# Optimization experiments

Measured on AMD Instinct MI355X. Metric: run time of the kernel, lower is better.

The kernel has to match this reference:

```python
import jax, jax.numpy as jnp
import numpy as np

D_MODEL = 1024
N_HEADS = 16
D_HEAD = D_MODEL // N_HEADS
D_FF = 4096
EPS = 1e-5


def layer_norm(x, g, b):
    mu = jnp.mean(x, axis=-1, keepdims=True)
    var = jnp.mean(jnp.square(x - mu), axis=-1, keepdims=True)
    return (x - mu) * jax.lax.rsqrt(var + EPS) * g + b


def setup_inputs() -> dict:
    key = jax.random.key(0)
    ks = jax.random.split(key, 8)
    s = 1.0 / np.sqrt(D_MODEL)
    return {
        "x": jax.random.normal(ks[0], (2, 2048, D_MODEL), dtype=jnp.float32),
        "Wq": jax.random.normal(ks[1], (N_HEADS, D_MODEL, D_HEAD), dtype=jnp.float32) * s,
        "Wk": jax.random.normal(ks[2], (N_HEADS, D_MODEL, D_HEAD), dtype=jnp.float32) * s,
        "Wv": jax.random.normal(ks[3], (N_HEADS, D_MODEL, D_HEAD), dtype=jnp.float32) * s,
        "Wo": jax.random.normal(ks[4], (D_MODEL, D_MODEL), dtype=jnp.float32) * s,
        "bo": jnp.zeros((D_MODEL,), dtype=jnp.float32),
        "ln1_g": jnp.ones((D_MODEL,), dtype=jnp.float32),
        "ln1_b": jnp.zeros((D_MODEL,), dtype=jnp.float32),
        "ln2_g": jnp.ones((D_MODEL,), dtype=jnp.float32),
        "ln2_b": jnp.zeros((D_MODEL,), dtype=jnp.float32),
        "W1": jax.random.normal(ks[5], (D_MODEL, D_FF), dtype=jnp.float32) * s,
        "b1": jnp.zeros((D_FF,), dtype=jnp.float32),
        "W2": jax.random.normal(ks[6], (D_FF, D_MODEL), dtype=jnp.float32) * (1.0 / np.sqrt(D_FF)),
        "b2": jnp.zeros((D_MODEL,), dtype=jnp.float32),
    }


def reference(x, Wq, Wk, Wv, Wo, bo, ln1_g, ln1_b, ln2_g, ln2_b, W1, b1, W2, b2):
    # Pre-norm MHA (per-head projections batched over head axis h)
    xn = layer_norm(x, ln1_g, ln1_b)
    q = jnp.einsum("bsd,hde->bhse", xn, Wq)
    k = jnp.einsum("bsd,hde->bhse", xn, Wk)
    v = jnp.einsum("bsd,hde->bhse", xn, Wv)
    scores = jnp.einsum("bhqe,bhke->bhqk", q, k) / jnp.sqrt(jnp.float32(D_HEAD))
    w = jax.nn.softmax(scores, axis=-1)
    attn = jnp.einsum("bhqk,bhke->bhqe", w, v)  # [b,h,s,dh]
    b, h, s, dh = attn.shape
    concat = attn.transpose(0, 2, 1, 3).reshape(b, s, h * dh)  # head concat order matches torch cat
    attn_out = concat @ Wo + bo
    hidden = x + attn_out
    hn = layer_norm(hidden, ln2_g, ln2_b)
    ff = jax.nn.gelu(hn @ W1 + b1, approximate=False) @ W2 + b2  # torch nn.GELU default = exact
    return hidden + ff
```

## Files before the change

kernel.cpp:

```cpp
#include <hip/hip_runtime.h>
#include <hip/hip_bf16.h>

typedef __bf16 bf16;
typedef __bf16 bf16x4 __attribute__((ext_vector_type(4)));
typedef __bf16 bf16x8 __attribute__((ext_vector_type(8)));
typedef float  f32x4  __attribute__((ext_vector_type(4)));

static __device__ __forceinline__ f32x4 mfma16(bf16x8 a, bf16x8 b, f32x4 c) {
  return __builtin_amdgcn_mfma_f32_16x16x32_bf16(a, b, c, 0, 0, 0);
}

static __device__ __forceinline__ float fexp2(float x) {
  return __builtin_amdgcn_exp2f(x);
}

static __device__ __forceinline__ void gl_lds16(const bf16* g, bf16* l) {
  __builtin_amdgcn_global_load_lds(
      (const __attribute__((address_space(1))) void*)g,
      (__attribute__((address_space(3))) void*)l, 16, 0, 0);
}

struct TrTab {
  const float* src[6];
  bf16* dst[6];
  int R[6], C[6], ntx[6], nty[6];
  int base[7];
};

__global__ __launch_bounds__(256) void tr6_kernel(TrTab tab) {
  int bid = blockIdx.x;
  int j = 0;
  while (j < 5 && bid >= tab.base[j + 1]) ++j;
  const int local = bid - tab.base[j];
  const int R = tab.R[j], C = tab.C[j];
  const int ntx = tab.ntx[j];
  const int per_z = ntx * tab.nty[j];
  const int z = local / per_z;
  const int rem = local - z * per_z;
  const int by = rem / ntx, bx = rem - by * ntx;
  const float* in = tab.src[j];
  bf16* out = tab.dst[j];

  __shared__ bf16 tile[32][33];
  const size_t zoff = (size_t)z * R * C;
  const int tx = threadIdx.x & 31, ty = threadIdx.x >> 5;
  const int x = bx * 32 + tx;
  const int y0 = by * 32;
#pragma unroll
  for (int jj = 0; jj < 4; ++jj)
    tile[ty + jj * 8][tx] = (bf16)in[zoff + (size_t)(y0 + ty + jj * 8) * C + x];
  __syncthreads();
  const int x2 = y0 + tx;
  const int y2 = bx * 32;
#pragma unroll
  for (int jj = 0; jj < 4; ++jj)
    out[zoff + (size_t)(y2 + ty + jj * 8) * R + x2] = tile[tx][ty + jj * 8];
}

__global__ __launch_bounds__(256) void trb_kernel(const bf16* __restrict__ inp,
                                                  bf16* __restrict__ out,
                                                  int R, int C) {
  __shared__ bf16 tile[32][33];
  const size_t zoff = (size_t)blockIdx.z * R * C;
  const int tx = threadIdx.x & 31, ty = threadIdx.x >> 5;
  const int x = blockIdx.x * 32 + tx;
  const int y0 = blockIdx.y * 32;
#pragma unroll
  for (int j = 0; j < 4; ++j)
    tile[ty + j * 8][tx] = inp[zoff + (size_t)(y0 + ty + j * 8) * C + x];
  __syncthreads();
  const int x2 = y0 + tx;
  const int y2 = blockIdx.x * 32;
#pragma unroll
  for (int j = 0; j < 4; ++j)
    out[zoff + (size_t)(y2 + ty + j * 8) * R + x2] = tile[tx][ty + j * 8];
}

__global__ __launch_bounds__(256) void ln_kernel(const float* __restrict__ inp,
                                                 const float* __restrict__ g,
                                                 const float* __restrict__ bt,
                                                 bf16* __restrict__ outp) {
  const int row = blockIdx.x;
  const int t = threadIdx.x;
  f32x4 v = ((const f32x4*)inp)[row * 256 + t];
  float s = v[0] + v[1] + v[2] + v[3];
  float sq = v[0] * v[0] + v[1] * v[1] + v[2] * v[2] + v[3] * v[3];
#pragma unroll
  for (int off = 32; off > 0; off >>= 1) {
    s += __shfl_xor(s, off);
    sq += __shfl_xor(sq, off);
  }
  __shared__ float red[8];
  const int wave = t >> 6, lane = t & 63;
  if (lane == 0) {
    red[wave] = s;
    red[wave + 4] = sq;
  }
  __syncthreads();
  s = red[0] + red[1] + red[2] + red[3];
  sq = red[4] + red[5] + red[6] + red[7];
  const float mu = s * (1.0f / 1024.0f);
  const float var = sq * (1.0f / 1024.0f) - mu * mu;
  const float rstd = rsqrtf(fmaxf(var, 0.0f) + 1e-5f);
  f32x4 gg = ((const f32x4*)g)[t];
  f32x4 bb = ((const f32x4*)bt)[t];
  bf16 o[4];
#pragma unroll
  for (int i = 0; i < 4; ++i)
    o[i] = (bf16)((v[i] - mu) * rstd * gg[i] + bb[i]);
  *(uint2*)&outp[(size_t)row * 1024 + 4 * t] = *(uint2*)o;
}

enum { EPI_QKV = 0, EPI_O = 1, EPI_FF1 = 2, EPI_FF2 = 3 };

#define VMW(N) asm volatile("s_waitcnt vmcnt(" #N ")" ::: "memory")
#define BARR                        \
  do {                              \
    __builtin_amdgcn_s_barrier();   \
    asm volatile("" ::: "memory");  \
  } while (0)

template <int EPI>
__global__ __launch_bounds__(512) void gemm256(
    const bf16* __restrict__ A, const bf16* __restrict__ Bt, const int K,
    const float* __restrict__ bias, bf16* __restrict__ outB) {
  __shared__ __align__(16) bf16 sA[2][256 * 64];
  __shared__ __align__(16) bf16 sB[2][256 * 64];
  const int t = threadIdx.x;
  const int lane = t & 63, wave = t >> 6;
  const int quad = lane >> 4, l15 = lane & 15;
  const int wm = wave >> 2, wn = wave & 3;
  const int m0 = blockIdx.y * 256, n0 = blockIdx.x * 256;
  const int srow = lane >> 3;
  const int scol = ((lane & 7) ^ srow) * 8;
  const int bch = (wave & 3) + (wave >> 2) * 8;

  const bf16* aS0 = A + (size_t)(m0 + wave * 8 + srow) * K + scol;
  const bf16* aS1 = aS0 + (size_t)64 * K;
  const bf16* bS0 = Bt + (size_t)(n0 + bch * 8 + srow) * K + scol;
  const bf16* bS1 = bS0 + (size_t)32 * K;
  const size_t rsk = (size_t)128 * K;

  auto stA0 = [&](int buf, int ko) {
    gl_lds16(aS0 + ko, &sA[buf][wave * 512]);
    gl_lds16(aS0 + ko + rsk, &sA[buf][(wave + 16) * 512]);
  };
  auto stB0 = [&](int buf, int ko) {
    gl_lds16(bS0 + ko, &sB[buf][bch * 512]);
    gl_lds16(bS0 + ko + rsk, &sB[buf][(bch + 16) * 512]);
  };
  auto stB1 = [&](int buf, int ko) {
    gl_lds16(bS1 + ko, &sB[buf][(bch + 4) * 512]);
    gl_lds16(bS1 + ko + rsk, &sB[buf][(bch + 20) * 512]);
  };
  auto stA1 = [&](int buf, int ko) {
    gl_lds16(aS1 + ko, &sA[buf][(wave + 8) * 512]);
    gl_lds16(aS1 + ko + rsk, &sA[buf][(wave + 24) * 512]);
  };

  f32x4 acc[8][4];
#pragma unroll
  for (int i = 0; i < 8; ++i)
#pragma unroll
    for (int j = 0; j < 4; ++j) acc[i][j] = {0.f, 0.f, 0.f, 0.f};

  bf16x8 af[4][2], bf0[2][2], bf1[2][2];

  auto ldA = [&](int buf, int mh) {
#pragma unroll
    for (int i = 0; i < 4; ++i) {
      const int row = wm * 128 + mh * 64 + i * 16 + l15;
#pragma unroll
      for (int ks = 0; ks < 2; ++ks) {
        const int col = ((ks * 4 + quad) ^ (row & 7)) * 8;
        af[i][ks] = *(const bf16x8*)&sA[buf][row * 64 + col];
      }
    }
  };
  auto ldB = [&](int buf, int nh, bf16x8 (&bfm)[2][2]) {
#pragma unroll
    for (int j = 0; j < 2; ++j) {
      const int row = wn * 64 + nh * 32 + j * 16 + l15;
#pragma unroll
      for (int ks = 0; ks < 2; ++ks) {
        const int col = ((ks * 4 + quad) ^ (row & 7)) * 8;
        bfm[j][ks] = *(const bf16x8*)&sB[buf][row * 64 + col];
      }
    }
  };
  auto mm = [&](int mh, int nh, bf16x8 (&bfm)[2][2]) {
    asm volatile("s_waitcnt lgkmcnt(0)" ::: "memory");
    __builtin_amdgcn_sched_barrier(0);
    __builtin_amdgcn_s_setprio(1);
#pragma unroll
    for (int ks = 0; ks < 2; ++ks)
#pragma unroll
      for (int i = 0; i < 4; ++i)
#pragma unroll
        for (int j = 0; j < 2; ++j)
          acc[mh * 4 + i][nh * 2 + j] =
              mfma16(af[i][ks], bfm[j][ks], acc[mh * 4 + i][nh * 2 + j]);
    __builtin_amdgcn_s_setprio(0);
    __builtin_amdgcn_sched_barrier(0);
  };

  stA0(0, 0);
  stB0(0, 0);
  stB1(0, 0);
  stA1(0, 0);

  const int NT = K >> 6;
#pragma unroll 1
  for (int it = 0; it < NT - 1; ++it) {
    const int cur = it & 1, nxt = cur ^ 1;
    const int ko = (it + 1) * 64;
    VMW(4);
    BARR;
    ldA(cur, 0);
    ldB(cur, 0, bf0);
    stA0(nxt, ko);
    mm(0, 0, bf0);
    VMW(4);
    BARR;
    ldB(cur, 1, bf1);
    stB0(nxt, ko);
    mm(0, 1, bf1);
    VMW(4);
    BARR;
    ldA(cur, 1);
    stB1(nxt, ko);
    mm(1, 1, bf1);
    ldB(cur, 0, bf0);
    stA1(nxt, ko);
    mm(1, 0, bf0);
  }
  {
    const int cur = (NT - 1) & 1;
    VMW(4);
    BARR;
    ldA(cur, 0);
    ldB(cur, 0, bf0);
    mm(0, 0, bf0);
    VMW(2);
    BARR;
    ldB(cur, 1, bf1);
    mm(0, 1, bf1);
    VMW(0);
    BARR;
    ldA(cur, 1);
    mm(1, 1, bf1);
    ldB(cur, 0, bf0);
    mm(1, 0, bf0);
  }

#pragma unroll
  for (int ni = 0; ni < 4; ++ni) {
    const int n = n0 + wn * 64 + ni * 16 + l15;
    float bv = 0.f;
    if constexpr (EPI == EPI_FF1) bv = bias[n];
#pragma unroll
    for (int mi = 0; mi < 8; ++mi) {
#pragma unroll
      for (int r = 0; r < 4; ++r) {
        const int m = m0 + wm * 128 + mi * 16 + quad * 4 + r;
        float v = acc[mi][ni][r];
        if constexpr (EPI == EPI_QKV) {
          const int which = n >> 10, nn = n & 1023;
          const int h = nn >> 6, e = nn & 63;
          const int b = m >> 11, s2 = m & 2047;
          outB[(size_t)which * 4194304 +
               ((size_t)(b * 16 + h) * 2048 + s2) * 64 + e] = (bf16)v;
        } else {
          v += bv;
          v = 0.5f * v * (1.0f + erff(v * 0.70710678118654752f));
          outB[(size_t)m * 4096 + n] = (bf16)v;
        }
      }
    }
  }
}

template <int EPI, bool NARROW>
__global__ __launch_bounds__(256) void gemm_bt(
    const bf16* __restrict__ A, const bf16* __restrict__ Bt, const int K,
    const float* __restrict__ bias, const float* __restrict__ res,
    bf16* __restrict__ outB, float* __restrict__ outF) {
  constexpr int BN = NARROW ? 64 : 128;
  constexpr int NI = NARROW ? 2 : 4;
  constexpr int BCH = BN / 32;
  __shared__ __align__(16) bf16 sA[2][128 * 64];
  __shared__ __align__(16) bf16 sB[2][BN * 64];
  const int t = threadIdx.x;
  const int lane = t & 63, wave = t >> 6;
  const int quad = lane >> 4, l15 = lane & 15;
  const int wr = wave >> 1, wc = wave & 1;
  const int m0 = blockIdx.y * 128, n0 = blockIdx.x * BN;
  const int srow = lane >> 3;
  const int scol = ((lane & 7) ^ srow) * 8;

  const bf16* aPtr[4];
#pragma unroll
  for (int c = 0; c < 4; ++c)
    aPtr[c] = A + (size_t)(m0 + wave * 32 + c * 8 + srow) * K + scol;
  const bf16* bPtr[BCH];
#pragma unroll
  for (int c = 0; c < BCH; ++c)
    bPtr[c] = Bt + (size_t)(n0 + wave * (BCH * 8) + c * 8 + srow) * K + scol;

  f32x4 acc[4][NI];
#pragma unroll
  for (int i = 0; i < 4; ++i)
#pragma unroll
    for (int j = 0; j < NI; ++j) acc[i][j] = {0.f, 0.f, 0.f, 0.f};

  const int niter = K >> 6;
#pragma unroll
  for (int c = 0; c < 4; ++c)
    gl_lds16(aPtr[c], &sA[0][(wave * 4 + c) * 512]);
#pragma unroll
  for (int c = 0; c < BCH; ++c)
    gl_lds16(bPtr[c], &sB[0][(wave * BCH + c) * 512]);

  for (int it = 0; it < niter; ++it) {
    const int cur = it & 1, nxt = cur ^ 1;
    __syncthreads();
    if (it + 1 < niter) {
      const int off = (it + 1) * 64;
#pragma unroll
      for (int c = 0; c < 4; ++c)
        gl_lds16(aPtr[c] + off, &sA[nxt][(wave * 4 + c) * 512]);
#pragma unroll
      for (int c = 0; c < BCH; ++c)
        gl_lds16(bPtr[c] + off, &sB[nxt][(wave * BCH + c) * 512]);
    }
#pragma unroll
    for (int ks = 0; ks < 2; ++ks) {
      bf16x8 af[4], bfr[NI];
#pragma unroll
      for (int mi = 0; mi < 4; ++mi) {
        const int row = wr * 64 + mi * 16 + l15;
        const int col = ((ks * 4 + quad) ^ (row & 7)) * 8;
        af[mi] = *(const bf16x8*)&sA[cur][row * 64 + col];
      }
#pragma unroll
      for (int ni = 0; ni < NI; ++ni) {
        const int row = wc * (BN / 2) + ni * 16 + l15;
        const int col = ((ks * 4 + quad) ^ (row & 7)) * 8;
        bfr[ni] = *(const bf16x8*)&sB[cur][row * 64 + col];
      }
#pragma unroll
      for (int mi = 0; mi < 4; ++mi)
#pragma unroll
        for (int ni = 0; ni < NI; ++ni)
          acc[mi][ni] = mfma16(af[mi], bfr[ni], acc[mi][ni]);
    }
  }

#pragma unroll
  for (int mi = 0; mi < 4; ++mi) {
#pragma unroll
    for (int ni = 0; ni < NI; ++ni) {
      const int n = n0 + wc * (BN / 2) + ni * 16 + l15;
#pragma unroll
      for (int r = 0; r < 4; ++r) {
        const int m = m0 + wr * 64 + mi * 16 + quad * 4 + r;
        float v = acc[mi][ni][r];
        if constexpr (EPI == EPI_QKV) {
          const int which = n >> 10, nn = n & 1023;
          const int h = nn >> 6, e = nn & 63;
          const int b = m >> 11, s2 = m & 2047;
          outB[(size_t)which * 4194304 +
               ((size_t)(b * 16 + h) * 2048 + s2) * 64 + e] = (bf16)v;
        } else if constexpr (EPI == EPI_O) {
          v += bias[n] + res[(size_t)m * 1024 + n];
          outF[(size_t)m * 1024 + n] = v;
        } else if constexpr (EPI == EPI_FF1) {
          v += bias[n];
          v = 0.5f * v * (1.0f + erff(v * 0.70710678118654752f));
          outB[(size_t)m * 4096 + n] = (bf16)v;
        } else {
          v += bias[n] + res[(size_t)m * 1024 + n];
          outF[(size_t)m * 1024 + n] = v;
        }
      }
    }
  }
}

__global__ __launch_bounds__(512, 4) void attn_kernel(
    const bf16* __restrict__ q, const bf16* __restrict__ k,
    const bf16* __restrict__ vt, bf16* __restrict__ ao) {
  __shared__ __align__(16) bf16 sP[256 * 72];
  __shared__ __align__(16) bf16 sK[2][64 * 64];
  __shared__ __align__(16) bf16 sV[2][64 * 64];
  const int t = threadIdx.x;
  const int lane = t & 63, wave = t >> 6;
  const int wq = wave & 3, kh = wave >> 2;
  const int quad = lane >> 4, l15 = lane & 15;
  const int q0 = blockIdx.x * 128;
  const int bh = blockIdx.y, b = bh >> 4, h = bh & 15;
  const bf16* Q  = q  + (size_t)bh * 2048 * 64;
  const bf16* Kp = k  + (size_t)bh * 2048 * 64 + (size_t)kh * 1024 * 64;
  const bf16* Vt = vt + (size_t)bh * 64 * 2048 + kh * 1024;
  const int srow = lane >> 3;
  const int scol = ((lane & 7) ^ srow) * 8;
  const float SCL = 0.125f * 1.4426950408889634f;

#pragma unroll
  for (int c = 0; c < 2; ++c) {
    const int chunk = wave * 2 + c;
    const int row = chunk * 8 + srow;
    gl_lds16(&Q[(size_t)(q0 + row) * 64 + scol], &sP[chunk * 512]);
  }
  __syncthreads();
  bf16x8 qf[2][2];
#pragma unroll
  for (int mi = 0; mi < 2; ++mi)
#pragma unroll
    for (int ks = 0; ks < 2; ++ks) {
      const int row = wq * 32 + mi * 16 + l15;
      const int col = ((ks * 4 + quad) ^ (row & 7)) * 8;
      qf[mi][ks] = *(const bf16x8*)&sP[row * 64 + col];
    }
  __syncthreads();

  f32x4 o[2][4];
  float ls[2] = {0.f, 0.f};
#pragma unroll
  for (int mi = 0; mi < 2; ++mi)
#pragma unroll
    for (int ne = 0; ne < 4; ++ne) o[mi][ne] = {0.f, 0.f, 0.f, 0.f};

  for (int kb = 0; kb < 16; ++kb) {
    const int kbase = kb * 64;
    __syncthreads();
#pragma unroll
    for (int c = 0; c < 2; ++c) {
      const int chunk = wq * 2 + c;
      const int row = chunk * 8 + srow;
      gl_lds16(&Kp[(size_t)(kbase + row) * 64 + scol], &sK[kh][chunk * 512]);
      gl_lds16(&Vt[(size_t)row * 2048 + kbase + scol], &sV[kh][chunk * 512]);
    }
    __syncthreads();

    f32x4 s[4][2];
#pragma unroll
    for (int ni = 0; ni < 4; ++ni)
#pragma unroll
      for (int mi = 0; mi < 2; ++mi) s[ni][mi] = {0.f, 0.f, 0.f, 0.f};
#pragma unroll
    for (int ks = 0; ks < 2; ++ks) {
      bf16x8 kf[4];
#pragma unroll
      for (int ni = 0; ni < 4; ++ni) {
        const int row = ni * 16 + l15;
        const int col = ((ks * 4 + quad) ^ (row & 7)) * 8;
        kf[ni] = *(const bf16x8*)&sK[kh][row * 64 + col];
      }
#pragma unroll
      for (int ni = 0; ni < 4; ++ni)
#pragma unroll
        for (int mi = 0; mi < 2; ++mi)
          s[ni][mi] = mfma16(kf[ni], qf[mi][ks], s[ni][mi]);
    }

#pragma unroll
    for (int mi = 0; mi < 2; ++mi)
#pragma unroll
      for (int ni = 0; ni < 4; ++ni) {
        bf16x4 p4;
#pragma unroll
        for (int r = 0; r < 4; ++r) {
          const float p = fexp2(s[ni][mi][r] * SCL);
          ls[mi] += p;
          p4[r] = (bf16)p;
        }
        *(bf16x4*)&sP[(wave * 32 + mi * 16 + l15) * 72 + ni * 16 + quad * 4] =
            p4;
      }

#pragma unroll
    for (int ksb = 0; ksb < 2; ++ksb) {
      bf16x8 vf[4];
#pragma unroll
      for (int ne = 0; ne < 4; ++ne) {
        const int row = ne * 16 + l15;
        const int col = ((ksb * 4 + quad) ^ (row & 7)) * 8;
        vf[ne] = *(const bf16x8*)&sV[kh][row * 64 + col];
      }
#pragma unroll
      for (int mi = 0; mi < 2; ++mi) {
        const bf16x8 pf = *(const bf16x8*)&sP[(wave * 32 + mi * 16 + l15) * 72 +
                                              ksb * 32 + quad * 8];
#pragma unroll
        for (int ne = 0; ne < 4; ++ne)
          o[mi][ne] = mfma16(pf, vf[ne], o[mi][ne]);
      }
    }
  }

#pragma unroll
  for (int mi = 0; mi < 2; ++mi) {
    ls[mi] += __shfl_xor(ls[mi], 16);
    ls[mi] += __shfl_xor(ls[mi], 32);
  }

  float* mo = (float*)sP;
  float* ml = (float*)sK;
  __syncthreads();
  if (kh == 1) {
    const int base = (wq * 64 + lane) * 32;
#pragma unroll
    for (int mi = 0; mi < 2; ++mi)
#pragma unroll
      for (int ne = 0; ne < 4; ++ne)
        *(f32x4*)&mo[base + (mi * 4 + ne) * 4] = o[mi][ne];
    ml[(wq * 64 + lane) * 2 + 0] = ls[0];
    ml[(wq * 64 + lane) * 2 + 1] = ls[1];
  }
  __syncthreads();
  if (kh == 0) {
    const int base = (wq * 64 + lane) * 32;
#pragma unroll
    for (int mi = 0; mi < 2; ++mi) {
#pragma unroll
      for (int ne = 0; ne < 4; ++ne) {
        const f32x4 add = *(const f32x4*)&mo[base + (mi * 4 + ne) * 4];
#pragma unroll
        for (int r = 0; r < 4; ++r) o[mi][ne][r] += add[r];
      }
      ls[mi] += ml[(wq * 64 + lane) * 2 + mi];
      ls[mi] = 1.0f / fmaxf(ls[mi], 1e-30f);
    }
#pragma unroll
    for (int mi = 0; mi < 2; ++mi) {
      float linv[4];
#pragma unroll
      for (int r = 0; r < 4; ++r) linv[r] = __shfl(ls[mi], quad * 4 + r);
#pragma unroll
      for (int ne = 0; ne < 4; ++ne)
#pragma unroll
        for (int r = 0; r < 4; ++r) {
          const int row = q0 + wq * 32 + mi * 16 + quad * 4 + r;
          const int col = h * 64 + ne * 16 + l15;
          ao[((size_t)(b * 2048 + row)) * 1024 + col] =
              (bf16)(o[mi][ne][r] * linv[r]);
        }
    }
  }
}

extern "C" void kernel_launch(void* const* d_in, const int* in_sizes, int n_in,
                              void* d_out, int out_size, void* d_ws,
                              size_t ws_size, hipStream_t stream) {
  const float* x    = (const float*)d_in[0];
  const float* Wq   = (const float*)d_in[1];
  const float* Wk   = (const float*)d_in[2];
  const float* Wv   = (const float*)d_in[3];
  const float* Wo   = (const float*)d_in[4];
  const float* bo   = (const float*)d_in[5];
  const float* ln1g = (const float*)d_in[6];
  const float* ln1b = (const float*)d_in[7];
  const float* ln2g = (const float*)d_in[8];
  const float* ln2b = (const float*)d_in[9];
  const float* W1   = (const float*)d_in[10];
  const float* b1   = (const float*)d_in[11];
  const float* W2   = (const float*)d_in[12];
  const float* b2   = (const float*)d_in[13];

  char* ws = (char*)d_ws;
  const size_t MB = 1ull << 20;
  bf16* QKVT = (bf16*)(ws);
  bf16* WqT  = QKVT;
  bf16* WkT  = (bf16*)(ws + 2 * MB);
  bf16* WvT  = (bf16*)(ws + 4 * MB);
  bf16* WoT  = (bf16*)(ws + 6 * MB);
  bf16* W1T  = (bf16*)(ws + 8 * MB);
  bf16* W2T  = (bf16*)(ws + 16 * MB);
  bf16* sh8  = (bf16*)(ws + 24 * MB);
  bf16* qb   = (bf16*)(ws + 32 * MB);
  bf16* kb   = (bf16*)(ws + 40 * MB);
  bf16* vb   = (bf16*)(ws + 48 * MB);
  bf16* vtb  = (bf16*)(ws + 56 * MB);
  bf16* h1   = (bf16*)(ws + 32 * MB);
  float* hid = (float*)(ws + 64 * MB);

  const dim3 blk(256);

  TrTab tab;
  const float* srcs[6] = {Wq, Wk, Wv, Wo, W1, W2};
  bf16* dsts[6] = {WqT, WkT, WvT, WoT, W1T, W2T};
  const int Rs[6] = {1024, 1024, 1024, 1024, 1024, 4096};
  const int Cs[6] = {64, 64, 64, 1024, 4096, 1024};
  const int Zs[6] = {16, 16, 16, 1, 1, 1};
  int base = 0;
  for (int j = 0; j < 6; ++j) {
    tab.src[j] = srcs[j];
    tab.dst[j] = dsts[j];
    tab.R[j] = Rs[j];
    tab.C[j] = Cs[j];
    tab.ntx[j] = Cs[j] / 32;
    tab.nty[j] = Rs[j] / 32;
    tab.base[j] = base;
    base += (Cs[j] / 32) * (Rs[j] / 32) * Zs[j];
  }
  tab.base[6] = base;
  tr6_kernel<<<base, blk, 0, stream>>>(tab);

  ln_kernel<<<4096, blk, 0, stream>>>(x, ln1g, ln1b, sh8);
  gemm256<EPI_QKV><<<dim3(12, 16), dim3(512), 0, stream>>>(
      sh8, QKVT, 1024, nullptr, qb);
  trb_kernel<<<dim3(2, 64, 32), blk, 0, stream>>>(vb, vtb, 2048, 64);
  attn_kernel<<<dim3(16, 32), dim3(512), 0, stream>>>(qb, kb, vtb, sh8);
  gemm_bt<EPI_O, true><<<dim3(16, 32), blk, 0, stream>>>(
      sh8, WoT, 1024, bo, x, nullptr, hid);
  ln_kernel<<<4096, blk, 0, stream>>>(hid, ln2g, ln2b, sh8);
  gemm256<EPI_FF1><<<dim3(16, 16), dim3(512), 0, stream>>>(
      sh8, W1T, 1024, b1, h1);
  gemm_bt<EPI_FF2, true><<<dim3(16, 32), blk, 0, stream>>>(
      h1, W2T, 4096, b2, hid, nullptr, (float*)d_out);

  (void)in_sizes; (void)n_in; (void)out_size; (void)ws_size;
}
```

Measured before the change: 364.1 us.

## Deepen gemm256 prefetch pipeline, add XCD-aware block swizzles, widen O-projection tile

Restructures the gemm256 main loop to prefetch two K-tiles ahead, issuing loads into the buffer just consumed and placing barriers around each MFMA phase instead of waiting on vmcnt at every phase. The peeled tail iteration is removed. Block indices in gemm256 and the attention kernel are remapped so that blocks landing on the same XCD share A/B tiles or heads for better L2 reuse. The O-projection switches to the wider 128-column gemm_bt variant with half the grid, and the epilogue loop order is changed so the bias is loaded once. The extra barriers and the two-ahead reuse of the current buffer add synchronisation cost and carry a risk of LDS hazards.

```diff
diff --git a/kernel.cpp b/kernel.cpp
--- a/kernel.cpp
+++ b/kernel.cpp
@@ -130,7 +130,14 @@
   const int lane = t & 63, wave = t >> 6;
   const int quad = lane >> 4, l15 = lane & 15;
   const int wm = wave >> 2, wn = wave & 3;
-  const int m0 = blockIdx.y * 256, n0 = blockIdx.x * 256;
+
+  const int gx = gridDim.x;
+  const int lin = blockIdx.y * gx + blockIdx.x;
+  const int xcd = lin & 7, idx = lin >> 3;
+  const int NBX = gx >> 1;
+  const int m0 = ((xcd & 3) * 4 + (idx & 3)) * 256;
+  const int n0 = ((xcd >> 2) * NBX + (idx >> 2)) * 256;
+
   const int srow = lane >> 3;
   const int scol = ((lane & 7) ^ srow) * 8;
   const int bch = (wave & 3) + (wave >> 2) * 8;
@@ -208,61 +215,57 @@
   stB0(0, 0);
   stB1(0, 0);
   stA1(0, 0);
+  stA0(1, 64);
+  stB0(1, 64);
+  stB1(1, 64);
+  VMW(6);
+  BARR;
 
   const int NT = K >> 6;
 #pragma unroll 1
-  for (int it = 0; it < NT - 1; ++it) {
+  for (int it = 0; it < NT; ++it) {
     const int cur = it & 1, nxt = cur ^ 1;
-    const int ko = (it + 1) * 64;
-    VMW(4);
-    BARR;
+    const int k1 = (it + 1) * 64, k2 = (it + 2) * 64;
     ldA(cur, 0);
     ldB(cur, 0, bf0);
-    stA0(nxt, ko);
+    if (it + 1 < NT) stA1(nxt, k1);
+    BARR;
     mm(0, 0, bf0);
-    VMW(4);
     BARR;
     ldB(cur, 1, bf1);
-    stB0(nxt, ko);
+    if (it + 2 < NT) stA0(cur, k2);
+    BARR;
     mm(0, 1, bf1);
-    VMW(4);
     BARR;
     ldA(cur, 1);
-    stB1(nxt, ko);
+    if (it + 2 < NT) stB0(cur, k2);
+    BARR;
     mm(1, 1, bf1);
-    ldB(cur, 0, bf0);
-    stA1(nxt, ko);
+    BARR;
+    if (it + 2 < NT) {
+      stB1(cur, k2);
+      VMW(6);
+    } else if (it + 1 < NT) {
+      VMW(0);
+    }
+    BARR;
     mm(1, 0, bf0);
-  }
-  {
-    const int cur = (NT - 1) & 1;
-    VMW(4);
-    BARR;
-    ldA(cur, 0);
-    ldB(cur, 0, bf0);
-    mm(0, 0, bf0);
-    VMW(2);
-    BARR;
-    ldB(cur, 1, bf1);
-    mm(0, 1, bf1);
-    VMW(0);
-    BARR;
-    ldA(cur, 1);
-    mm(1, 1, bf1);
-    ldB(cur, 0, bf0);
-    mm(1, 0, bf0);
-  }
-
-#pragma unroll
-  for (int ni = 0; ni < 4; ++ni) {
-    const int n = n0 + wn * 64 + ni * 16 + l15;
-    float bv = 0.f;
-    if constexpr (EPI == EPI_FF1) bv = bias[n];
-#pragma unroll
-    for (int mi = 0; mi < 8; ++mi) {
-#pragma unroll
-      for (int r = 0; r < 4; ++r) {
-        const int m = m0 + wm * 128 + mi * 16 + quad * 4 + r;
+    BARR;
+  }
+
+  float bv4[4] = {0.f, 0.f, 0.f, 0.f};
+  if constexpr (EPI == EPI_FF1) {
+#pragma unroll
+    for (int ni = 0; ni < 4; ++ni) bv4[ni] = bias[n0 + wn * 64 + ni * 16 + l15];
+  }
+#pragma unroll
+  for (int mi = 0; mi < 8; ++mi) {
+#pragma unroll
+    for (int r = 0; r < 4; ++r) {
+      const int m = m0 + wm * 128 + mi * 16 + quad * 4 + r;
+#pragma unroll
+      for (int ni = 0; ni < 4; ++ni) {
+        const int n = n0 + wn * 64 + ni * 16 + l15;
         float v = acc[mi][ni][r];
         if constexpr (EPI == EPI_QKV) {
           const int which = n >> 10, nn = n & 1023;
@@ -271,7 +274,7 @@
           outB[(size_t)which * 4194304 +
                ((size_t)(b * 16 + h) * 2048 + s2) * 64 + e] = (bf16)v;
         } else {
-          v += bv;
+          v += bv4[ni];
           v = 0.5f * v * (1.0f + erff(v * 0.70710678118654752f));
           outB[(size_t)m * 4096 + n] = (bf16)v;
         }
@@ -397,8 +400,12 @@
   const int lane = t & 63, wave = t >> 6;
   const int wq = wave & 3, kh = wave >> 2;
   const int quad = lane >> 4, l15 = lane & 15;
-  const int q0 = blockIdx.x * 128;
-  const int bh = blockIdx.y, b = bh >> 4, h = bh & 15;
+
+  const int lin = blockIdx.y * 16 + blockIdx.x;
+  const int sw = (lin & 7) * 64 + (lin >> 3);
+  const int q0 = (sw & 15) * 128;
+  const int bh = sw >> 4, b = bh >> 4, h = bh & 15;
+
   const bf16* Q  = q  + (size_t)bh * 2048 * 64;
   const bf16* Kp = k  + (size_t)bh * 2048 * 64 + (size_t)kh * 1024 * 64;
   const bf16* Vt = vt + (size_t)bh * 64 * 2048 + kh * 1024;
@@ -612,7 +619,7 @@
       sh8, QKVT, 1024, nullptr, qb);
   trb_kernel<<<dim3(2, 64, 32), blk, 0, stream>>>(vb, vtb, 2048, 64);
   attn_kernel<<<dim3(16, 32), dim3(512), 0, stream>>>(qb, kb, vtb, sh8);
-  gemm_bt<EPI_O, true><<<dim3(16, 32), blk, 0, stream>>>(
+  gemm_bt<EPI_O, false><<<dim3(8, 32), blk, 0, stream>>>(
       sh8, WoT, 1024, bo, x, nullptr, hid);
   ln_kernel<<<4096, blk, 0, stream>>>(hid, ln2g, ln2b, sh8);
   gemm256<EPI_FF1><<<dim3(16, 16), dim3(512), 0, stream>>>(
```

After: 356.0 us (median of 3 runs). 2.2% less time.
